# Optimization experiments

Hardware: AMD Instinct MI355X
Metric: run time of the kernel (lower is better)

## Reference

```python
import jax, jax.numpy as jnp
import numpy as np

B, IN_CH, OUT_CH, N_MAPS, H, W_DIM, CTRL = 64, 32, 32, 64, 64, 64, 512
NF = N_MAPS                # forget gate units
NI = IN_CH * N_MAPS       # input gate units
NO = OUT_CH * N_MAPS      # output gate units


def setup_inputs() -> dict:
    key = jax.random.key(0)
    k1, k2, k3, k4 = jax.random.split(key, 4)
    inputs = jax.random.normal(k1, (B, IN_CH, H, W_DIM), dtype=jnp.float32)
    state = jax.random.normal(k2, (B, N_MAPS, H, W_DIM), dtype=jnp.float32)
    controls = jax.random.normal(k3, (B, CTRL), dtype=jnp.float32)
    Wc = jax.random.normal(k4, (NF + NI + NO, CTRL), dtype=jnp.float32) * (CTRL ** -0.5)
    return {"inputs": inputs, "state": state, "controls": controls, "W": Wc}


def reference(inputs, state, controls, W):
    # control linear (no bias): [B, NF+NI+NO]
    ctrl = controls @ W.T
    f = ctrl[:, :NF]                         # [B, n_maps]
    i = ctrl[:, NF:NF + NI]                  # [B, in_ch*n_maps]
    o = ctrl[:, NF + NI:]                    # [B, out_ch*n_maps]
    in_gates = i.reshape(B, N_MAPS, IN_CH)   # per-sample 1x1 conv filters
    forget_gates = f.reshape(B, N_MAPS, 1, 1)
    out_gates = o.reshape(B, OUT_CH, N_MAPS)
    # per-sample 1x1 conv == batched channel contraction
    gated_inputs = jnp.einsum('bchw,bmc->bmhw', inputs, in_gates)
    new_state = gated_inputs + state * forget_gates
    output = jnp.tanh(new_state)
    outputs = jnp.einsum('bmhw,bom->bohw', output, out_gates)
    return (outputs, new_state)
```

## Files before the change

### kernel.cpp

```cpp
#include <hip/hip_runtime.h>
#include <cstdint>
#include <cstddef>

#define B_SZ   64
#define IN_CH  32
#define OUT_CH 32
#define NMAPS  64
#define HW     4096
#define CTRLN  512
#define NROWS  4160
#define OUT0_SZ (B_SZ*OUT_CH*HW)
#define TILE   128


__device__ __forceinline__ float fast_tanh(float x) {
    float e = __expf(2.0f * x);
    return 1.0f - 2.0f * __builtin_amdgcn_rcpf(e + 1.0f);
}

__global__ __launch_bounds__(256) void ctrl_gemm(
    const float* __restrict__ controls, const float* __restrict__ W,
    float* __restrict__ ws)
{
    const int tid = threadIdx.x;
    const int b   = tid & 63;
    const int w   = __builtin_amdgcn_readfirstlane(tid >> 6);
    const int j0  = blockIdx.x * 16 + w * 4;

    const float4* cb = (const float4*)(controls + b * CTRLN);
    const float*  w0 = W + (size_t)j0 * CTRLN;

    float acc[4] = {0.f, 0.f, 0.f, 0.f};
#pragma unroll 4
    for (int kk = 0; kk < CTRLN / 4; ++kk) {
        float4 x = cb[kk];
#pragma unroll
        for (int r = 0; r < 4; ++r) {
            float4 wv = *(const float4*)(w0 + r * CTRLN + kk * 4);
            acc[r] += wv.x * x.x + wv.y * x.y + wv.z * x.z + wv.w * x.w;
        }
    }
    float* wb = ws + (size_t)b * NROWS + j0;
#pragma unroll
    for (int r = 0; r < 4; ++r) wb[r] = acc[r];
}

__global__ __launch_bounds__(256, 3) void vstm_main(
    const float* __restrict__ inputs, const float* __restrict__ state,
    const float* __restrict__ ws, float* __restrict__ out)
{
    __shared__ __align__(16) float uni[64 * TILE];
    __shared__ __align__(16) float igs[32 * 68];
    __shared__ __align__(16) float ogs[64 * 36];
    __shared__ __align__(16) float fs[64];

    const int tid  = threadIdx.x;
    const int b    = blockIdx.y;
    const int tile = blockIdx.x * TILE;
    const int tx   = tid & 63;
    const int wy   = __builtin_amdgcn_readfirstlane(tid >> 6);

    const float* g = ws + (size_t)b * NROWS;
    if (tid < 64) fs[tid] = g[tid];
#pragma unroll
    for (int i = 0; i < 8; ++i) {
        const int idx = i * 256 + tid;
        igs[(idx & 31) * 68 + (idx >> 5)] = g[64 + idx];
        ogs[(idx & 63) * 36 + (idx >> 6)] = g[2112 + idx];
    }

    const float* inb = inputs + (size_t)b * IN_CH * HW + tile;
    float4* Xs4 = (float4*)uni;
#pragma unroll
    for (int i = 0; i < 4; ++i) {
        const int idx = i * 256 + tid;
        const int c = idx >> 5, p4 = idx & 31;
        Xs4[c * 32 + p4] = *(const float4*)(inb + c * HW + p4 * 4);
    }
    __syncthreads();

    const int m0 = wy * 16;
    float acc0[16], acc1[16];
#pragma unroll
    for (int j = 0; j < 16; ++j) { acc0[j] = 0.f; acc1[j] = 0.f; }

#pragma unroll 8
    for (int c = 0; c < IN_CH; ++c) {
        const float x0 = uni[c * TILE + tx];
        const float x1 = uni[c * TILE + 64 + tx];
        float gg[16];
        const float4* gp = (const float4*)&igs[c * 68 + m0];
        *(float4*)&gg[0]  = gp[0];
        *(float4*)&gg[4]  = gp[1];
        *(float4*)&gg[8]  = gp[2];
        *(float4*)&gg[12] = gp[3];
#pragma unroll
        for (int j = 0; j < 16; ++j) {
            acc0[j] += gg[j] * x0;
            acc1[j] += gg[j] * x1;
        }
    }

    float fr[16];
    *(float4*)&fr[0]  = *(const float4*)&fs[m0];
    *(float4*)&fr[4]  = *(const float4*)&fs[m0 + 4];
    *(float4*)&fr[8]  = *(const float4*)&fs[m0 + 8];
    *(float4*)&fr[12] = *(const float4*)&fs[m0 + 12];

    const float* stb = state + (size_t)b * NMAPS * HW + tile;
    float*       nsb = out + OUT0_SZ + (size_t)b * NMAPS * HW + tile;
    float t0[16], t1[16];
#pragma unroll
    for (int j = 0; j < 16; ++j) {
        const int m = m0 + j;
        const float ns0 = acc0[j] + stb[m * HW + tx]      * fr[j];
        const float ns1 = acc1[j] + stb[m * HW + 64 + tx] * fr[j];
        nsb[m * HW + tx]      = ns0;
        nsb[m * HW + 64 + tx] = ns1;
        t0[j] = fast_tanh(ns0);
        t1[j] = fast_tanh(ns1);
    }
    __syncthreads();

#pragma unroll
    for (int j = 0; j < 16; ++j) {
        uni[(m0 + j) * TILE + tx]      = t0[j];
        uni[(m0 + j) * TILE + 64 + tx] = t1[j];
    }
    __syncthreads();

    const int o0 = wy * 8;
    float bacc0[8], bacc1[8];
#pragma unroll
    for (int j = 0; j < 8; ++j) { bacc0[j] = 0.f; bacc1[j] = 0.f; }

#pragma unroll 8
    for (int m = 0; m < NMAPS; ++m) {
        const float u0 = uni[m * TILE + tx];
        const float u1 = uni[m * TILE + 64 + tx];
        float og[8];
        *(float4*)&og[0] = *(const float4*)&ogs[m * 36 + o0];
        *(float4*)&og[4] = *(const float4*)&ogs[m * 36 + o0 + 4];
#pragma unroll
        for (int j = 0; j < 8; ++j) {
            bacc0[j] += og[j] * u0;
            bacc1[j] += og[j] * u1;
        }
    }

    float* ob = out + (size_t)b * OUT_CH * HW + tile;
#pragma unroll
    for (int j = 0; j < 8; ++j) {
        ob[(o0 + j) * HW + tx]      = bacc0[j];
        ob[(o0 + j) * HW + 64 + tx] = bacc1[j];
    }
}

extern "C" void kernel_launch(void* const* d_in, const int* in_sizes, int n_in,
                              void* d_out, int out_size, void* d_ws, size_t ws_size,
                              hipStream_t stream) {
    const float* inputs   = (const float*)d_in[0];
    const float* state    = (const float*)d_in[1];
    const float* controls = (const float*)d_in[2];
    const float* W        = (const float*)d_in[3];
    float*       out      = (float*)d_out;
    float*       ws       = (float*)d_ws;

    ctrl_gemm<<<dim3(NROWS / 16), 256, 0, stream>>>(controls, W, ws);

    dim3 g2(HW / TILE, B_SZ);
    vstm_main<<<g2, 256, 0, stream>>>(inputs, state, ws, out);
}
```

Before: 228.2 us.

## Use bf16 MFMA for both per-sample channel contractions and transpose controls via LDS

Both einsum contractions in the main kernel now run on the 16x16x32 bf16 MFMA instruction instead of scalar FMAs. Inputs, gates and tanh outputs are rounded to bf16 and staged transposed in LDS, and occupancy launch bounds rise from 3 to 4 blocks per CU. The control GEMM now stages a transposed control tile in shared memory and reads W as scalars rather than float4 rows. Rounding to bf16 lowers precision, and the per-element global loads and stores in the MFMA output layout coalesce in 16-lane runs instead of full 64-lane runs.

```diff
diff --git a/kernel.cpp b/kernel.cpp
--- a/kernel.cpp
+++ b/kernel.cpp
@@ -12,7 +12,13 @@
 #define OUT0_SZ (B_SZ*OUT_CH*HW)
 #define TILE   128
 
+typedef short bf8_t  __attribute__((ext_vector_type(8)));
+typedef float f32x4  __attribute__((ext_vector_type(4)));
 
+__device__ __forceinline__ unsigned short f2bf(float f) {
+    union { float f; uint32_t u; } v; v.f = f;
+    return (unsigned short)((v.u + 0x7FFFu + ((v.u >> 16) & 1u)) >> 16);
+}
 __device__ __forceinline__ float fast_tanh(float x) {
     float e = __expf(2.0f * x);
     return 1.0f - 2.0f * __builtin_amdgcn_rcpf(e + 1.0f);
@@ -22,22 +28,34 @@
     const float* __restrict__ controls, const float* __restrict__ W,
     float* __restrict__ ws)
 {
+    __shared__ __align__(16) float ct[128 * 65];
     const int tid = threadIdx.x;
     const int b   = tid & 63;
     const int w   = __builtin_amdgcn_readfirstlane(tid >> 6);
     const int j0  = blockIdx.x * 16 + w * 4;
-
-    const float4* cb = (const float4*)(controls + b * CTRLN);
-    const float*  w0 = W + (size_t)j0 * CTRLN;
+    const float* w0 = W + (size_t)j0 * CTRLN;
 
     float acc[4] = {0.f, 0.f, 0.f, 0.f};
+    for (int kc = 0; kc < CTRLN; kc += 128) {
+        __syncthreads();
+#pragma unroll
+        for (int i = 0; i < 8; ++i) {
+            const int flat = (i * 256 + tid) * 4;
+            const int bb = flat >> 7;
+            const int kk = flat & 127;
+            float4 v = *(const float4*)(controls + (size_t)bb * CTRLN + kc + kk);
+            ct[(kk + 0) * 65 + bb] = v.x;
+            ct[(kk + 1) * 65 + bb] = v.y;
+            ct[(kk + 2) * 65 + bb] = v.z;
+            ct[(kk + 3) * 65 + bb] = v.w;
+        }
+        __syncthreads();
 #pragma unroll 4
-    for (int kk = 0; kk < CTRLN / 4; ++kk) {
-        float4 x = cb[kk];
+        for (int k = 0; k < 128; ++k) {
+            const float c = ct[k * 65 + b];
 #pragma unroll
-        for (int r = 0; r < 4; ++r) {
-            float4 wv = *(const float4*)(w0 + r * CTRLN + kk * 4);
-            acc[r] += wv.x * x.x + wv.y * x.y + wv.z * x.z + wv.w * x.w;
+            for (int r = 0; r < 4; ++r)
+                acc[r] += w0[r * CTRLN + kc + k] * c;
         }
     }
     float* wb = ws + (size_t)b * NROWS + j0;
@@ -45,114 +63,97 @@
     for (int r = 0; r < 4; ++r) wb[r] = acc[r];
 }
 
-__global__ __launch_bounds__(256, 3) void vstm_main(
+__global__ __launch_bounds__(256, 4) void vstm_main(
     const float* __restrict__ inputs, const float* __restrict__ state,
     const float* __restrict__ ws, float* __restrict__ out)
 {
-    __shared__ __align__(16) float uni[64 * TILE];
-    __shared__ __align__(16) float igs[32 * 68];
-    __shared__ __align__(16) float ogs[64 * 36];
+    __shared__ __align__(16) unsigned short Xt[TILE * 40];
+    __shared__ __align__(16) unsigned short IGs[64 * 40];
+    __shared__ __align__(16) unsigned short OGs[32 * 72];
+    __shared__ __align__(16) unsigned short Tt[TILE * 72];
     __shared__ __align__(16) float fs[64];
 
     const int tid  = threadIdx.x;
     const int b    = blockIdx.y;
     const int tile = blockIdx.x * TILE;
-    const int tx   = tid & 63;
-    const int wy   = __builtin_amdgcn_readfirstlane(tid >> 6);
+    const int w    = __builtin_amdgcn_readfirstlane(tid >> 6);
+    const int l    = tid & 63;
+    const int lhi  = l >> 4;
+    const int llo  = l & 15;
 
     const float* g = ws + (size_t)b * NROWS;
     if (tid < 64) fs[tid] = g[tid];
 #pragma unroll
     for (int i = 0; i < 8; ++i) {
         const int idx = i * 256 + tid;
-        igs[(idx & 31) * 68 + (idx >> 5)] = g[64 + idx];
-        ogs[(idx & 63) * 36 + (idx >> 6)] = g[2112 + idx];
+        IGs[(idx >> 5) * 40 + (idx & 31)] = f2bf(g[64 + idx]);
+        OGs[(idx >> 6) * 72 + (idx & 63)] = f2bf(g[2112 + idx]);
     }
-
     const float* inb = inputs + (size_t)b * IN_CH * HW + tile;
-    float4* Xs4 = (float4*)uni;
 #pragma unroll
-    for (int i = 0; i < 4; ++i) {
-        const int idx = i * 256 + tid;
-        const int c = idx >> 5, p4 = idx & 31;
-        Xs4[c * 32 + p4] = *(const float4*)(inb + c * HW + p4 * 4);
+    for (int i = 0; i < 16; ++i) {
+        const int flat = i * 256 + tid;
+        const int c = flat >> 7, p = flat & 127;
+        Xt[p * 40 + c] = f2bf(inb[c * HW + p]);
     }
     __syncthreads();
 
-    const int m0 = wy * 16;
-    float acc0[16], acc1[16];
+    const bf8_t af = *(const bf8_t*)&IGs[(w * 16 + llo) * 40 + lhi * 8];
+    f32x4 acc[8];
 #pragma unroll
-    for (int j = 0; j < 16; ++j) { acc0[j] = 0.f; acc1[j] = 0.f; }
-
-#pragma unroll 8
-    for (int c = 0; c < IN_CH; ++c) {
-        const float x0 = uni[c * TILE + tx];
-        const float x1 = uni[c * TILE + 64 + tx];
-        float gg[16];
-        const float4* gp = (const float4*)&igs[c * 68 + m0];
-        *(float4*)&gg[0]  = gp[0];
-        *(float4*)&gg[4]  = gp[1];
-        *(float4*)&gg[8]  = gp[2];
-        *(float4*)&gg[12] = gp[3];
-#pragma unroll
-        for (int j = 0; j < 16; ++j) {
-            acc0[j] += gg[j] * x0;
-            acc1[j] += gg[j] * x1;
-        }
+    for (int pc = 0; pc < 8; ++pc) {
+        acc[pc] = (f32x4){0.f, 0.f, 0.f, 0.f};
+        const bf8_t bf = *(const bf8_t*)&Xt[(pc * 16 + llo) * 40 + lhi * 8];
+        acc[pc] = __builtin_amdgcn_mfma_f32_16x16x32_bf16(af, bf, acc[pc], 0, 0, 0);
     }
 
-    float fr[16];
-    *(float4*)&fr[0]  = *(const float4*)&fs[m0];
-    *(float4*)&fr[4]  = *(const float4*)&fs[m0 + 4];
-    *(float4*)&fr[8]  = *(const float4*)&fs[m0 + 8];
-    *(float4*)&fr[12] = *(const float4*)&fs[m0 + 12];
+    float fr[4];
+#pragma unroll
+    for (int r = 0; r < 4; ++r) fr[r] = fs[w * 16 + lhi * 4 + r];
 
     const float* stb = state + (size_t)b * NMAPS * HW + tile;
     float*       nsb = out + OUT0_SZ + (size_t)b * NMAPS * HW + tile;
-    float t0[16], t1[16];
 #pragma unroll
-    for (int j = 0; j < 16; ++j) {
-        const int m = m0 + j;
-        const float ns0 = acc0[j] + stb[m * HW + tx]      * fr[j];
-        const float ns1 = acc1[j] + stb[m * HW + 64 + tx] * fr[j];
-        nsb[m * HW + tx]      = ns0;
-        nsb[m * HW + 64 + tx] = ns1;
-        t0[j] = fast_tanh(ns0);
-        t1[j] = fast_tanh(ns1);
+    for (int pc = 0; pc < 8; ++pc) {
+        const int p = pc * 16 + llo;
+#pragma unroll
+        for (int r = 0; r < 4; ++r) {
+            const int m = w * 16 + lhi * 4 + r;
+            const float ns = acc[pc][r] + stb[m * HW + p] * fr[r];
+            nsb[m * HW + p] = ns;
+            Tt[p * 72 + m] = f2bf(fast_tanh(ns));
+        }
     }
     __syncthreads();
 
+    const int oc  = w >> 1;
+    const int pcb = (w & 1) * 4;
+    bf8_t ag[2];
 #pragma unroll
-    for (int j = 0; j < 16; ++j) {
-        uni[(m0 + j) * TILE + tx]      = t0[j];
-        uni[(m0 + j) * TILE + 64 + tx] = t1[j];
-    }
-    __syncthreads();
+    for (int ks = 0; ks < 2; ++ks)
+        ag[ks] = *(const bf8_t*)&OGs[(oc * 16 + llo) * 72 + ks * 32 + lhi * 8];
 
-    const int o0 = wy * 8;
-    float bacc0[8], bacc1[8];
+    f32x4 acc2[4];
 #pragma unroll
-    for (int j = 0; j < 8; ++j) { bacc0[j] = 0.f; bacc1[j] = 0.f; }
-
-#pragma unroll 8
-    for (int m = 0; m < NMAPS; ++m) {
-        const float u0 = uni[m * TILE + tx];
-        const float u1 = uni[m * TILE + 64 + tx];
-        float og[8];
-        *(float4*)&og[0] = *(const float4*)&ogs[m * 36 + o0];
-        *(float4*)&og[4] = *(const float4*)&ogs[m * 36 + o0 + 4];
+    for (int t = 0; t < 4; ++t) {
+        acc2[t] = (f32x4){0.f, 0.f, 0.f, 0.f};
+        const int pc = pcb + t;
 #pragma unroll
-        for (int j = 0; j < 8; ++j) {
-            bacc0[j] += og[j] * u0;
-            bacc1[j] += og[j] * u1;
+        for (int ks = 0; ks < 2; ++ks) {
+            const bf8_t bt = *(const bf8_t*)&Tt[(pc * 16 + llo) * 72 + ks * 32 + lhi * 8];
+            acc2[t] = __builtin_amdgcn_mfma_f32_16x16x32_bf16(ag[ks], bt, acc2[t], 0, 0, 0);
         }
     }
 
     float* ob = out + (size_t)b * OUT_CH * HW + tile;
 #pragma unroll
-    for (int j = 0; j < 8; ++j) {
-        ob[(o0 + j) * HW + tx]      = bacc0[j];
-        ob[(o0 + j) * HW + 64 + tx] = bacc1[j];
+    for (int t = 0; t < 4; ++t) {
+        const int p = (pcb + t) * 16 + llo;
+#pragma unroll
+        for (int r = 0; r < 4; ++r) {
+            const int o = oc * 16 + lhi * 4 + r;
+            ob[o * HW + p] = acc2[t][r];
+        }
     }
 }
 
```

Result: no change. 227.8 us (-0.2%).
